# Optimization experiments

Measured on AMD Instinct MI355X. Metric: run time of the kernel, lower is better.

The kernel has to match this reference:

```python
import jax, jax.numpy as jnp
import numpy as np

N_HEADS = 32
N_KV_HEADS = 8
HEAD_DIM = 128
ROPE_BASE = 10000.0
NEG_INF = -1e9


def rope(x, base=ROPE_BASE, offset=0):
    # x: [B, H, L, d]; 'traditional' RoPE with the module's rotation formula.
    d = x.shape[-1]
    t = jnp.arange(x.shape[2], dtype=jnp.float32) + offset
    freqs = base ** (-jnp.arange(0, d, 2, dtype=jnp.float32) / d)  # [d/2]
    ang = t[:, None] * freqs[None, :]                              # [L, d/2]
    cos, sin = jnp.cos(ang), jnp.sin(ang)
    x1, x2 = x[..., 0::2], x[..., 1::2]
    out = jnp.stack([x1 * cos + x2 * sin, x1 * sin - x2 * cos], axis=-1)
    return out.reshape(x.shape)


def setup_inputs() -> dict:
    key = jax.random.key(0)
    ks = jax.random.split(key, 5)
    B, L, D = 2, 2048, 4096
    x = jax.random.normal(ks[0], (B, L, D), dtype=jnp.float32)
    wq = jax.random.normal(ks[1], (D, N_HEADS * HEAD_DIM), dtype=jnp.float32) * 0.02
    wk = jax.random.normal(ks[2], (D, N_KV_HEADS * HEAD_DIM), dtype=jnp.float32) * 0.02
    wv = jax.random.normal(ks[3], (D, N_KV_HEADS * HEAD_DIM), dtype=jnp.float32) * 0.02
    wo = jax.random.normal(ks[4], (N_HEADS * HEAD_DIM, D), dtype=jnp.float32) * 0.02
    # causal additive mask [L, L]
    mask = jnp.where(jnp.tril(jnp.ones((L, L), dtype=bool)), 0.0, NEG_INF).astype(jnp.float32)
    return {"x": x, "mask": mask, "wq": wq, "wk": wk, "wv": wv, "wo": wo}


def reference(x, mask, wq, wk, wv, wo):
    B, L, D = x.shape
    scale = HEAD_DIM ** -0.5
    q = (x @ wq).reshape(B, L, N_HEADS, HEAD_DIM).transpose(0, 2, 1, 3)     # [B,H,L,d]
    k = (x @ wk).reshape(B, L, N_KV_HEADS, HEAD_DIM).transpose(0, 2, 1, 3)  # [B,Hk,L,d]
    v = (x @ wv).reshape(B, L, N_KV_HEADS, HEAD_DIM).transpose(0, 2, 1, 3)
    rep = N_HEADS // N_KV_HEADS
    k = jnp.repeat(k, rep, axis=1)  # [B,H,L,d]  (physical GQA repeat, as in source)
    v = jnp.repeat(v, rep, axis=1)
    q = rope(q)
    k = rope(k)
    scores = jnp.einsum("bhqd,bhkd->bhqk", q * scale, k) + mask  # [B,H,L,L]
    probs = jax.nn.softmax(scores.astype(jnp.float32), axis=-1).astype(scores.dtype)
    out = jnp.einsum("bhqk,bhkd->bhqd", probs, v)
    out = out.transpose(0, 2, 1, 3).reshape(B, L, N_HEADS * HEAD_DIM)
    return out @ wo, (k, v)
```

## Files before the change

kernel.cpp:

```cpp
#include <hip/hip_runtime.h>

typedef unsigned short u16;
typedef unsigned int u32;
typedef float f32x4 __attribute__((ext_vector_type(4)));
typedef u32 u32x2 __attribute__((ext_vector_type(2)));
typedef __bf16 bf16x8 __attribute__((ext_vector_type(8)));

#define DEV __device__ __forceinline__

DEV u16 f2b(float f) {
    union { float f; u32 u; } v; v.f = f;
    u32 r = v.u + 0x7fffu + ((v.u >> 16) & 1u);
    return (u16)(r >> 16);
}
DEV float b2f(u16 b) {
    union { u32 u; float f; } v; v.u = ((u32)b) << 16;
    return v.f;
}

DEV void gload16(const void* g, void* l) {
    __builtin_amdgcn_global_load_lds((const __attribute__((address_space(1))) void*)g,
                                     (__attribute__((address_space(3))) void*)l, 16, 0, 0);
}

DEV f32x4 mfma16(bf16x8 a, bf16x8 b, f32x4 c) {
    return __builtin_amdgcn_mfma_f32_16x16x32_bf16(a, b, c, 0, 0, 0);
}

__global__ __launch_bounds__(256) void convx_kernel(const float* __restrict__ in,
                                                    u16* __restrict__ out) {
    size_t i = ((size_t)blockIdx.x * 256 + threadIdx.x) * 4;
    float4 v = *(const float4*)(in + i);
    ushort4 o; o.x = f2b(v.x); o.y = f2b(v.y); o.z = f2b(v.z); o.w = f2b(v.w);
    *(ushort4*)(out + i) = o;
}

__global__ __launch_bounds__(256) void tconv3_kernel(const float* __restrict__ wq,
                                                     const float* __restrict__ wk,
                                                     const float* __restrict__ wv,
                                                     u16* __restrict__ out) {
    __shared__ float tile[64][65];
    int t = threadIdx.x;
    int n0 = blockIdx.x * 64, k0 = blockIdx.y * 64;
    const float* src; int Ns, nl;
    if (n0 < 4096)      { src = wq; Ns = 4096; nl = n0; }
    else if (n0 < 5120) { src = wk; Ns = 1024; nl = n0 - 4096; }
    else                { src = wv; Ns = 1024; nl = n0 - 5120; }
    int r = t >> 4, c4 = (t & 15) * 4;
#pragma unroll
    for (int i = 0; i < 4; ++i) {
        float4 v = *(const float4*)(src + (size_t)(k0 + i * 16 + r) * Ns + nl + c4);
        tile[i * 16 + r][c4 + 0] = v.x; tile[i * 16 + r][c4 + 1] = v.y;
        tile[i * 16 + r][c4 + 2] = v.z; tile[i * 16 + r][c4 + 3] = v.w;
    }
    __syncthreads();
#pragma unroll
    for (int i = 0; i < 4; ++i) {
        int nn = i * 16 + r;
        ushort4 o;
        o.x = f2b(tile[c4 + 0][nn]); o.y = f2b(tile[c4 + 1][nn]);
        o.z = f2b(tile[c4 + 2][nn]); o.w = f2b(tile[c4 + 3][nn]);
        *(ushort4*)(out + (size_t)(n0 + nn) * 4096 + k0 + c4) = o;
    }
}

__global__ __launch_bounds__(256) void tconv_kernel(const float* __restrict__ in,
                                                    u16* __restrict__ out, int K, int N) {
    __shared__ float tile[64][65];
    int t = threadIdx.x;
    int n0 = blockIdx.x * 64, k0 = blockIdx.y * 64;
    int r = t >> 4, c4 = (t & 15) * 4;
#pragma unroll
    for (int i = 0; i < 4; ++i) {
        float4 v = *(const float4*)(in + (size_t)(k0 + i * 16 + r) * N + n0 + c4);
        tile[i * 16 + r][c4 + 0] = v.x; tile[i * 16 + r][c4 + 1] = v.y;
        tile[i * 16 + r][c4 + 2] = v.z; tile[i * 16 + r][c4 + 3] = v.w;
    }
    __syncthreads();
#pragma unroll
    for (int i = 0; i < 4; ++i) {
        int nn = i * 16 + r;
        ushort4 o;
        o.x = f2b(tile[c4 + 0][nn]); o.y = f2b(tile[c4 + 1][nn]);
        o.z = f2b(tile[c4 + 2][nn]); o.w = f2b(tile[c4 + 3][nn]);
        *(ushort4*)(out + (size_t)(n0 + nn) * K + k0 + c4) = o;
    }
}

#define GEMM128_BODY                                                                        \
    __shared__ __align__(16) u16 Asb[2][2][64 * 64];                                        \
    __shared__ __align__(16) u16 Bsb[2][2][64 * 64];                                        \
    int t = threadIdx.x;                                                                    \
    int lane = t & 63, w = t >> 6;                                                          \
    int wrM = w >> 1, wcN = w & 1;                                                          \
    int lr = lane & 15, hi = lane >> 4;                                                     \
    int wg = blockIdx.x;                                                                    \
    int swz = (wg & 7) * ((int)gridDim.x >> 3) + (wg >> 3);                                 \
    int bx = swz / gy, by = swz % gy;                                                       \
    int m0 = by * 128, n0 = bx * 128;                                                       \
    int nk = K >> 6;                                                                        \
    auto stageA = [&](int X, int h) {                                                       \
        const u16* src = A + (size_t)(m0 + h * 64) * K + X * 64;                            \
        char* dst = (char*)&Asb[X & 1][h][0];                                               \
        _Pragma("unroll")                                                                   \
        for (int it = 0; it < 2; ++it) {                                                    \
            int c = it * 256 + t;                                                           \
            int row = c >> 3;                                                               \
            int col8 = ((c & 7) ^ (row & 7)) << 3;                                          \
            gload16(src + (size_t)row * K + col8, dst + (it * 256 + (t & ~63)) * 16);       \
        }                                                                                   \
    };                                                                                      \
    auto stageB = [&](int X, int h) {                                                       \
        const u16* src = Bt + (size_t)(n0 + h * 64) * K + X * 64;                           \
        char* dst = (char*)&Bsb[X & 1][h][0];                                               \
        _Pragma("unroll")                                                                   \
        for (int it = 0; it < 2; ++it) {                                                    \
            int c = it * 256 + t;                                                           \
            int row = c >> 3;                                                               \
            int col8 = ((c & 7) ^ (row & 7)) << 3;                                          \
            gload16(src + (size_t)row * K + col8, dst + (it * 256 + (t & ~63)) * 16);       \
        }                                                                                   \
    };                                                                                      \
    stageA(0, 0); stageA(0, 1); stageB(0, 0); stageB(0, 1);                                 \
    stageA(1, 0); stageA(1, 1);                                                             \
    asm volatile("s_waitcnt vmcnt(4)" ::: "memory");                                        \
    __builtin_amdgcn_s_barrier();                                                           \
    f32x4 acc[4][4] = {};                                                                   \
    for (int kt = 0; kt < nk; ++kt) {                                                       \
        __builtin_amdgcn_sched_barrier(0);                                                  \
        int p = kt & 1;                                                                     \
        const char* Ah = (const char*)&Asb[p][wrM][0];                                      \
        const char* Bh = (const char*)&Bsb[p][wcN][0];                                      \
        bool s1 = (kt + 1 < nk), s2 = (kt + 2 < nk);                                        \
        bf16x8 a[4][2], bb[2][2];                                                           \
        _Pragma("unroll")                                                                   \
        for (int mf = 0; mf < 4; ++mf)                                                      \
            _Pragma("unroll")                                                               \
            for (int ks = 0; ks < 2; ++ks) {                                                \
                int row = mf * 16 + lr;                                                     \
                a[mf][ks] = *(const bf16x8*)(Ah + ((row * 128 + ks * 64 + hi * 16) ^ ((row & 7) << 4))); \
            }                                                                               \
        _Pragma("unroll")                                                                   \
        for (int nf = 0; nf < 2; ++nf)                                                      \
            _Pragma("unroll")                                                               \
            for (int ks = 0; ks < 2; ++ks) {                                                \
                int row = nf * 16 + lr;                                                     \
                bb[nf][ks] = *(const bf16x8*)(Bh + ((row * 128 + ks * 64 + hi * 16) ^ ((row & 7) << 4))); \
            }                                                                               \
        if (s1) { stageB(kt + 1, 0); stageB(kt + 1, 1); }                                   \
        __builtin_amdgcn_s_barrier();                                                       \
        __builtin_amdgcn_s_setprio(1);                                                      \
        _Pragma("unroll")                                                                   \
        for (int mf = 0; mf < 4; ++mf)                                                      \
            _Pragma("unroll")                                                               \
            for (int nf = 0; nf < 2; ++nf)                                                  \
                _Pragma("unroll")                                                           \
                for (int ks = 0; ks < 2; ++ks)                                              \
                    acc[mf][nf] = mfma16(a[mf][ks], bb[nf][ks], acc[mf][nf]);               \
        __builtin_amdgcn_s_setprio(0);                                                      \
        __builtin_amdgcn_s_barrier();                                                       \
        _Pragma("unroll")                                                                   \
        for (int nf = 0; nf < 2; ++nf)                                                      \
            _Pragma("unroll")                                                               \
            for (int ks = 0; ks < 2; ++ks) {                                                \
                int row = (nf + 2) * 16 + lr;                                               \
                bb[nf][ks] = *(const bf16x8*)(Bh + ((row * 128 + ks * 64 + hi * 16) ^ ((row & 7) << 4))); \
            }                                                                               \
        if (s2) { stageA(kt + 2, 0); stageA(kt + 2, 1); }                                   \
        __builtin_amdgcn_s_barrier();                                                       \
        __builtin_amdgcn_s_setprio(1);                                                      \
        _Pragma("unroll")                                                                   \
        for (int mf = 0; mf < 4; ++mf)                                                      \
            _Pragma("unroll")                                                               \
            for (int nf = 0; nf < 2; ++nf)                                                  \
                _Pragma("unroll")                                                           \
                for (int ks = 0; ks < 2; ++ks)                                              \
                    acc[mf][nf + 2] = mfma16(a[mf][ks], bb[nf][ks], acc[mf][nf + 2]);       \
        __builtin_amdgcn_s_setprio(0);                                                      \
        if (s2)      asm volatile("s_waitcnt vmcnt(4)" ::: "memory");                       \
        else if (s1) asm volatile("s_waitcnt vmcnt(0)" ::: "memory");                       \
        __builtin_amdgcn_s_barrier();                                                       \
    }

__global__ __launch_bounds__(256, 2) void gemm128_bf16_kernel(const u16* __restrict__ A,
                                                              const u16* __restrict__ Bt,
                                                              u16* __restrict__ Cb,
                                                              int N, int K, int gy) {
    GEMM128_BODY
#pragma unroll
    for (int mf = 0; mf < 4; ++mf)
#pragma unroll
        for (int nf = 0; nf < 4; ++nf)
#pragma unroll
            for (int r = 0; r < 4; ++r) {
                int m = m0 + wrM * 64 + mf * 16 + hi * 4 + r;
                int n = n0 + wcN * 64 + nf * 16 + lr;
                Cb[(size_t)m * N + n] = f2b(acc[mf][nf][r]);
            }
}

__global__ __launch_bounds__(256, 2) void gemm128_f32_kernel(const u16* __restrict__ A,
                                                             const u16* __restrict__ Bt,
                                                             float* __restrict__ Cf,
                                                             int N, int K, int gy) {
    GEMM128_BODY
#pragma unroll
    for (int mf = 0; mf < 4; ++mf)
#pragma unroll
        for (int nf = 0; nf < 4; ++nf)
#pragma unroll
            for (int r = 0; r < 4; ++r) {
                int m = m0 + wrM * 64 + mf * 16 + hi * 4 + r;
                int n = n0 + wcN * 64 + nf * 16 + lr;
                Cf[(size_t)m * N + n] = acc[mf][nf][r];
            }
}

__global__ __launch_bounds__(256) void postproc_kernel(u16* __restrict__ qkv,
                                                       float* __restrict__ outk,
                                                       u16* __restrict__ vt,
                                                       float* __restrict__ outv) {
    int id = blockIdx.x;
    int tid = threadIdx.x;
    if (id < 40960) {
        int row = id / 10;
        int p = (id % 10) * 256 + tid;
        int b = row >> 11, l = row & 2047;
        float freq = exp2f((float)(p & 63) * -0.2076205059304601f);
        float sv, cv; sincosf((float)l * freq, &sv, &cv);
        if (p < 2048) {
            int h = p >> 6, i = p & 63;
            size_t idx = (size_t)row * 6144 + h * 128 + 2 * i;
            u32 pr = *(const u32*)(qkv + idx);
            float x1 = b2f((u16)(pr & 0xffff)), x2 = b2f((u16)(pr >> 16));
            float o1 = x1 * cv + x2 * sv, o2 = x1 * sv - x2 * cv;
            *(u32*)(qkv + idx) = (u32)f2b(o1) | ((u32)f2b(o2) << 16);
        } else {
            int kvh = (p >> 6) - 32, i = p & 63;
            size_t idx = (size_t)row * 6144 + 4096 + kvh * 128 + 2 * i;
            u32 pr = *(const u32*)(qkv + idx);
            float x1 = b2f((u16)(pr & 0xffff)), x2 = b2f((u16)(pr >> 16));
            float o1 = x1 * cv + x2 * sv, o2 = x1 * sv - x2 * cv;
            *(u32*)(qkv + idx) = (u32)f2b(o1) | ((u32)f2b(o2) << 16);
#pragma unroll
            for (int r = 0; r < 4; ++r) {
                float2 o; o.x = o1; o.y = o2;
                *(float2*)(outk + ((size_t)((b * 32 + kvh * 4 + r) * 2048) + l) * 128 + 2 * i) = o;
            }
        }
    } else {
        __shared__ u16 tile[64][65];
        int i0 = id - 40960;
        int l0 = (i0 & 31) * 64, d0 = ((i0 >> 5) & 1) * 64;
        int z = i0 >> 6, b = z >> 3, kvh = z & 7;
        int r = tid >> 4, c4 = (tid & 15) * 4;
#pragma unroll
        for (int i = 0; i < 4; ++i) {
            int l = l0 + i * 16 + r;
            ushort4 v = *(const ushort4*)(qkv + (size_t)(b * 2048 + l) * 6144 + 5120 + kvh * 128 + d0 + c4);
            tile[i * 16 + r][c4 + 0] = v.x; tile[i * 16 + r][c4 + 1] = v.y;
            tile[i * 16 + r][c4 + 2] = v.z; tile[i * 16 + r][c4 + 3] = v.w;
            float4 f; f.x = b2f(v.x); f.y = b2f(v.y); f.z = b2f(v.z); f.w = b2f(v.w);
#pragma unroll
            for (int rr = 0; rr < 4; ++rr)
                *(float4*)(outv + ((size_t)((b * 32 + kvh * 4 + rr) * 2048) + l) * 128 + d0 + c4) = f;
        }
        __syncthreads();
#pragma unroll
        for (int i = 0; i < 4; ++i) {
            int dn = i * 16 + r;
            ushort4 o;
            o.x = tile[c4 + 0][dn]; o.y = tile[c4 + 1][dn];
            o.z = tile[c4 + 2][dn]; o.w = tile[c4 + 3][dn];
            *(ushort4*)(vt + (size_t)((b * 8 + kvh) * 128 + d0 + dn) * 2048 + l0 + c4) = o;
        }
    }
}

__global__ __launch_bounds__(256, 2) void attn_kernel(const u16* __restrict__ qkv,
                                                      const u16* __restrict__ vt,
                                                      u16* __restrict__ ab) {
    __shared__ __align__(16) u16 Kbuf[2][64 * 128];
    __shared__ __align__(16) u16 Vbuf[2][128 * 64];
    __shared__ __align__(16) u16 Ps[4][32 * 64];
    int t = threadIdx.x, lane = t & 63, w = t >> 6;
    int lr = lane & 15, hi = lane >> 4;
    int h = blockIdx.y, b = blockIdx.z, kvh = h >> 2;

    const u16* kbase = qkv + (size_t)(b * 2048) * 6144 + 4096 + kvh * 128;
    const u16* vtbase = vt + (size_t)((b * 8 + kvh) * 128) * 2048;

    auto stageKV = [&](int k0, int buf) {
#pragma unroll
        for (int i = 0; i < 4; ++i) {
            int c = i * 256 + t;
            int row = c >> 4;
            int col8 = ((c & 15) ^ (row & 7)) << 3;
            gload16(kbase + (size_t)(k0 + row) * 6144 + col8,
                    (char*)Kbuf[buf] + (i * 256 + (t & ~63)) * 16);
        }
#pragma unroll
        for (int i = 0; i < 4; ++i) {
            int c = i * 256 + t;
            int row = c >> 3;
            int col8 = ((c & 7) ^ (row & 7)) << 3;
            gload16(vtbase + (size_t)row * 2048 + k0 + col8,
                    (char*)Vbuf[buf] + (i * 256 + (t & ~63)) * 16);
        }
    };

    auto process = [&](int qblk) {
        int q0 = qblk * 128;
        bf16x8 qf[2][4];
#pragma unroll
        for (int half = 0; half < 2; ++half)
#pragma unroll
            for (int kki = 0; kki < 4; ++kki)
                qf[half][kki] = *(const bf16x8*)(qkv +
                    (size_t)(b * 2048 + q0 + w * 32 + half * 16 + lr) * 6144 + h * 128 +
                    kki * 32 + 8 * hi);
        f32x4 acc[2][8] = {};
        float mrun[2] = {-1e30f, -1e30f}, lrun[2] = {0.f, 0.f};

        int nt = 2 * (qblk + 1);
        stageKV(0, 0);
        __syncthreads();
        int cur = 0;
        for (int kt = 0; kt < nt; ++kt) {
            if (kt + 1 < nt) stageKV((kt + 1) * 64, cur ^ 1);
            __builtin_amdgcn_sched_barrier(0);

            const u16* Ks = Kbuf[cur];
            const u16* Vs = Vbuf[cur];
            f32x4 s[2][4] = {};
            __builtin_amdgcn_s_setprio(1);
#pragma unroll
            for (int kki = 0; kki < 4; ++kki) {
                bf16x8 kf[4];
#pragma unroll
                for (int fc = 0; fc < 4; ++fc) {
                    int kvr = fc * 16 + lr;
                    int byt = (kvr * 256 + (kki * 32 + 8 * hi) * 2) ^ ((kvr & 7) << 4);
                    kf[fc] = *(const bf16x8*)((const char*)Ks + byt);
                }
#pragma unroll
                for (int fc = 0; fc < 4; ++fc) {
                    s[0][fc] = mfma16(kf[fc], qf[0][kki], s[0][fc]);
                    s[1][fc] = mfma16(kf[fc], qf[1][kki], s[1][fc]);
                }
            }
            __builtin_amdgcn_s_setprio(0);
            const float SC = 0.08838834764831845f;
            int domask = (kt >= nt - 2);
            u16* Pw = Ps[w];
#pragma unroll
            for (int half = 0; half < 2; ++half) {
                int qabs = q0 + w * 32 + half * 16 + lr;
#pragma unroll
                for (int fc = 0; fc < 4; ++fc)
#pragma unroll
                    for (int r = 0; r < 4; ++r) {
                        float v = s[half][fc][r] * SC;
                        if (domask && (kt * 64 + fc * 16 + hi * 4 + r) > qabs) v = -1e30f;
                        s[half][fc][r] = v;
                    }
                float pm = s[half][0][0];
#pragma unroll
                for (int fc = 0; fc < 4; ++fc)
#pragma unroll
                    for (int r = 0; r < 4; ++r) pm = fmaxf(pm, s[half][fc][r]);
                pm = fmaxf(pm, __shfl_xor(pm, 16));
                pm = fmaxf(pm, __shfl_xor(pm, 32));
                float mn = fmaxf(mrun[half], pm);
                float fr = __expf(mrun[half] - mn);
                mrun[half] = mn;
                float ls = 0.f;
#pragma unroll
                for (int fc = 0; fc < 4; ++fc)
#pragma unroll
                    for (int r = 0; r < 4; ++r) {
                        float e = __expf(s[half][fc][r] - mn);
                        s[half][fc][r] = e;
                        ls += e;
                    }
                ls += __shfl_xor(ls, 16);
                ls += __shfl_xor(ls, 32);
                lrun[half] = lrun[half] * fr + ls;
#pragma unroll
                for (int dhf = 0; dhf < 8; ++dhf)
#pragma unroll
                    for (int r = 0; r < 4; ++r) acc[half][dhf][r] *= fr;
#pragma unroll
                for (int fc = 0; fc < 4; ++fc) {
                    u32x2 pk;
                    pk.x = (u32)f2b(s[half][fc][0]) | ((u32)f2b(s[half][fc][1]) << 16);
                    pk.y = (u32)f2b(s[half][fc][2]) | ((u32)f2b(s[half][fc][3]) << 16);
                    int byt = (half * 2048 + lr * 128 + fc * 32 + hi * 8) ^ ((lr & 7) << 4);
                    *(u32x2*)((char*)Pw + byt) = pk;
                }
            }
            asm volatile("s_waitcnt lgkmcnt(0)" ::: "memory");
            __builtin_amdgcn_s_setprio(1);
#pragma unroll
            for (int kk2 = 0; kk2 < 2; ++kk2) {
                bf16x8 pf0 = *(const bf16x8*)((const char*)Pw +
                    ((lr * 128 + kk2 * 64 + hi * 16) ^ ((lr & 7) << 4)));
                bf16x8 pf1 = *(const bf16x8*)((const char*)Pw +
                    ((2048 + lr * 128 + kk2 * 64 + hi * 16) ^ ((lr & 7) << 4)));
#pragma unroll
                for (int dhf = 0; dhf < 8; ++dhf) {
                    int dh = dhf * 16 + lr;
                    int bytv = (dh * 128 + (kk2 * 32 + 8 * hi) * 2) ^ ((dh & 7) << 4);
                    bf16x8 vf = *(const bf16x8*)((const char*)Vs + bytv);
                    acc[0][dhf] = mfma16(vf, pf0, acc[0][dhf]);
                    acc[1][dhf] = mfma16(vf, pf1, acc[1][dhf]);
                }
            }
            __builtin_amdgcn_s_setprio(0);
            __syncthreads();
            cur ^= 1;
        }
#pragma unroll
        for (int half = 0; half < 2; ++half) {
            float inv = 1.0f / lrun[half];
            int qrow = q0 + w * 32 + half * 16 + lr;
#pragma unroll
            for (int dhf = 0; dhf < 8; ++dhf) {
                ushort4 o;
                o.x = f2b(acc[half][dhf][0] * inv); o.y = f2b(acc[half][dhf][1] * inv);
                o.z = f2b(acc[half][dhf][2] * inv); o.w = f2b(acc[half][dhf][3] * inv);
                *(ushort4*)(ab + (size_t)(b * 2048 + qrow) * 4096 + h * 128 + dhf * 16 + hi * 4) = o;
            }
        }
    };

    process(15 - blockIdx.x);
    __syncthreads();
    process(blockIdx.x);
}

extern "C" void kernel_launch(void* const* d_in, const int* in_sizes, int n_in,
                              void* d_out, int out_size, void* d_ws, size_t ws_size,
                              hipStream_t stream) {
    (void)in_sizes; (void)n_in; (void)out_size; (void)ws_size;
    const float* x  = (const float*)d_in[0];
    const float* wq = (const float*)d_in[2];
    const float* wk = (const float*)d_in[3];
    const float* wv = (const float*)d_in[4];
    const float* wo = (const float*)d_in[5];

    char* ws = (char*)d_ws;
    u16* xb  = (u16*)(ws + 0);
    u16* fBt = (u16*)(ws + 33554432);
    u16* qkv = (u16*)(ws + 83886080);
    u16* vt  = (u16*)(ws + 134217728);
    u16* ab  = xb;
    u16* wob = fBt;

    float* out0 = (float*)d_out;
    float* outk = out0 + 16777216;
    float* outv = out0 + 33554432;

    convx_kernel<<<16384, 256, 0, stream>>>(x, xb);
    tconv3_kernel<<<dim3(96, 64), 256, 0, stream>>>(wq, wk, wv, fBt);

    gemm128_bf16_kernel<<<1536, 256, 0, stream>>>(xb, fBt, qkv, 6144, 4096, 32);

    tconv_kernel<<<dim3(64, 64), 256, 0, stream>>>(wo, wob, 4096, 4096);

    postproc_kernel<<<41984, 256, 0, stream>>>(qkv, outk, vt, outv);

    attn_kernel<<<dim3(8, 32, 2), 256, 0, stream>>>(qkv, vt, ab);

    gemm128_f32_kernel<<<1024, 256, 0, stream>>>(ab, wob, out0, 4096, 4096, 32);
}
```

Before: 580.9 us.

## Merge preprocessing kernels, fold softmax scale into Q RoPE, add lazy rescaling

Folds the x conversion, the QKV weight transpose and the wo transpose into one preproc kernel, which removes three launches and lets the wo conversion run before the QKV GEMM. wo gets its own workspace region so it no longer aliases fBt. The attention scale is applied to Q during RoPE postprocessing instead of per score tile. The online softmax now rescales the accumulators only when the running max grows by more than a threshold, which cuts per-tile multiplies at some risk to numeric range.

```diff
diff --git a/kernel.cpp b/kernel.cpp
--- a/kernel.cpp
+++ b/kernel.cpp
@@ -27,25 +27,36 @@
     return __builtin_amdgcn_mfma_f32_16x16x32_bf16(a, b, c, 0, 0, 0);
 }
 
-__global__ __launch_bounds__(256) void convx_kernel(const float* __restrict__ in,
-                                                    u16* __restrict__ out) {
-    size_t i = ((size_t)blockIdx.x * 256 + threadIdx.x) * 4;
-    float4 v = *(const float4*)(in + i);
-    ushort4 o; o.x = f2b(v.x); o.y = f2b(v.y); o.z = f2b(v.z); o.w = f2b(v.w);
-    *(ushort4*)(out + i) = o;
-}
-
-__global__ __launch_bounds__(256) void tconv3_kernel(const float* __restrict__ wq,
-                                                     const float* __restrict__ wk,
-                                                     const float* __restrict__ wv,
-                                                     u16* __restrict__ out) {
+__global__ __launch_bounds__(256) void preproc_kernel(const float* __restrict__ x,
+                                                      const float* __restrict__ wq,
+                                                      const float* __restrict__ wk,
+                                                      const float* __restrict__ wv,
+                                                      const float* __restrict__ wo,
+                                                      u16* __restrict__ xb,
+                                                      u16* __restrict__ fBt,
+                                                      u16* __restrict__ wob) {
+    int id = blockIdx.x;
+    int t = threadIdx.x;
+    if (id < 16384) {
+        size_t i = ((size_t)id * 256 + t) * 4;
+        float4 v = *(const float4*)(x + i);
+        ushort4 o; o.x = f2b(v.x); o.y = f2b(v.y); o.z = f2b(v.z); o.w = f2b(v.w);
+        *(ushort4*)(xb + i) = o;
+        return;
+    }
     __shared__ float tile[64][65];
-    int t = threadIdx.x;
-    int n0 = blockIdx.x * 64, k0 = blockIdx.y * 64;
-    const float* src; int Ns, nl;
-    if (n0 < 4096)      { src = wq; Ns = 4096; nl = n0; }
-    else if (n0 < 5120) { src = wk; Ns = 1024; nl = n0 - 4096; }
-    else                { src = wv; Ns = 1024; nl = n0 - 5120; }
+    const float* src; u16* dst; int Ns, nl, n0, k0, Kst;
+    if (id < 22528) {
+        int i0 = id - 16384;
+        n0 = (i0 % 96) * 64; k0 = (i0 / 96) * 64; Kst = 4096; dst = fBt;
+        if (n0 < 4096)      { src = wq; Ns = 4096; nl = n0; }
+        else if (n0 < 5120) { src = wk; Ns = 1024; nl = n0 - 4096; }
+        else                { src = wv; Ns = 1024; nl = n0 - 5120; }
+    } else {
+        int i1 = id - 22528;
+        n0 = (i1 & 63) * 64; k0 = (i1 >> 6) * 64; Kst = 4096; dst = wob;
+        src = wo; Ns = 4096; nl = n0;
+    }
     int r = t >> 4, c4 = (t & 15) * 4;
 #pragma unroll
     for (int i = 0; i < 4; ++i) {
@@ -60,30 +71,7 @@
         ushort4 o;
         o.x = f2b(tile[c4 + 0][nn]); o.y = f2b(tile[c4 + 1][nn]);
         o.z = f2b(tile[c4 + 2][nn]); o.w = f2b(tile[c4 + 3][nn]);
-        *(ushort4*)(out + (size_t)(n0 + nn) * 4096 + k0 + c4) = o;
-    }
-}
-
-__global__ __launch_bounds__(256) void tconv_kernel(const float* __restrict__ in,
-                                                    u16* __restrict__ out, int K, int N) {
-    __shared__ float tile[64][65];
-    int t = threadIdx.x;
-    int n0 = blockIdx.x * 64, k0 = blockIdx.y * 64;
-    int r = t >> 4, c4 = (t & 15) * 4;
-#pragma unroll
-    for (int i = 0; i < 4; ++i) {
-        float4 v = *(const float4*)(in + (size_t)(k0 + i * 16 + r) * N + n0 + c4);
-        tile[i * 16 + r][c4 + 0] = v.x; tile[i * 16 + r][c4 + 1] = v.y;
-        tile[i * 16 + r][c4 + 2] = v.z; tile[i * 16 + r][c4 + 3] = v.w;
-    }
-    __syncthreads();
-#pragma unroll
-    for (int i = 0; i < 4; ++i) {
-        int nn = i * 16 + r;
-        ushort4 o;
-        o.x = f2b(tile[c4 + 0][nn]); o.y = f2b(tile[c4 + 1][nn]);
-        o.z = f2b(tile[c4 + 2][nn]); o.w = f2b(tile[c4 + 3][nn]);
-        *(ushort4*)(out + (size_t)(n0 + nn) * K + k0 + c4) = o;
+        *(ushort4*)(dst + (size_t)(n0 + nn) * Kst + k0 + c4) = o;
     }
 }
 
@@ -229,11 +217,12 @@
         float freq = exp2f((float)(p & 63) * -0.2076205059304601f);
         float sv, cv; sincosf((float)l * freq, &sv, &cv);
         if (p < 2048) {
+            const float SC = 0.08838834764831845f;
             int h = p >> 6, i = p & 63;
             size_t idx = (size_t)row * 6144 + h * 128 + 2 * i;
             u32 pr = *(const u32*)(qkv + idx);
             float x1 = b2f((u16)(pr & 0xffff)), x2 = b2f((u16)(pr >> 16));
-            float o1 = x1 * cv + x2 * sv, o2 = x1 * sv - x2 * cv;
+            float o1 = (x1 * cv + x2 * sv) * SC, o2 = (x1 * sv - x2 * cv) * SC;
             *(u32*)(qkv + idx) = (u32)f2b(o1) | ((u32)f2b(o2) << 16);
         } else {
             int kvh = (p >> 6) - 32, i = p & 63;
@@ -350,20 +339,18 @@
                 }
             }
             __builtin_amdgcn_s_setprio(0);
-            const float SC = 0.08838834764831845f;
             int domask = (kt >= nt - 2);
             u16* Pw = Ps[w];
 #pragma unroll
             for (int half = 0; half < 2; ++half) {
                 int qabs = q0 + w * 32 + half * 16 + lr;
-#pragma unroll
-                for (int fc = 0; fc < 4; ++fc)
-#pragma unroll
-                    for (int r = 0; r < 4; ++r) {
-                        float v = s[half][fc][r] * SC;
-                        if (domask && (kt * 64 + fc * 16 + hi * 4 + r) > qabs) v = -1e30f;
-                        s[half][fc][r] = v;
-                    }
+                if (domask) {
+#pragma unroll
+                    for (int fc = 0; fc < 4; ++fc)
+#pragma unroll
+                        for (int r = 0; r < 4; ++r)
+                            if ((kt * 64 + fc * 16 + hi * 4 + r) > qabs) s[half][fc][r] = -1e30f;
+                }
                 float pm = s[half][0][0];
 #pragma unroll
                 for (int fc = 0; fc < 4; ++fc)
@@ -371,25 +358,28 @@
                     for (int r = 0; r < 4; ++r) pm = fmaxf(pm, s[half][fc][r]);
                 pm = fmaxf(pm, __shfl_xor(pm, 16));
                 pm = fmaxf(pm, __shfl_xor(pm, 32));
-                float mn = fmaxf(mrun[half], pm);
-                float fr = __expf(mrun[half] - mn);
-                mrun[half] = mn;
+                if (!__all(pm - mrun[half] <= 8.0f)) {
+                    float mn = fmaxf(mrun[half], pm);
+                    float fr = __expf(mrun[half] - mn);
+                    mrun[half] = mn;
+                    lrun[half] *= fr;
+#pragma unroll
+                    for (int dhf = 0; dhf < 8; ++dhf)
+#pragma unroll
+                        for (int r = 0; r < 4; ++r) acc[half][dhf][r] *= fr;
+                }
                 float ls = 0.f;
 #pragma unroll
                 for (int fc = 0; fc < 4; ++fc)
 #pragma unroll
                     for (int r = 0; r < 4; ++r) {
-                        float e = __expf(s[half][fc][r] - mn);
+                        float e = __expf(s[half][fc][r] - mrun[half]);
                         s[half][fc][r] = e;
                         ls += e;
                     }
                 ls += __shfl_xor(ls, 16);
                 ls += __shfl_xor(ls, 32);
-                lrun[half] = lrun[half] * fr + ls;
-#pragma unroll
-                for (int dhf = 0; dhf < 8; ++dhf)
-#pragma unroll
-                    for (int r = 0; r < 4; ++r) acc[half][dhf][r] *= fr;
+                lrun[half] += ls;
 #pragma unroll
                 for (int fc = 0; fc < 4; ++fc) {
                     u32x2 pk;
@@ -455,19 +445,15 @@
     u16* qkv = (u16*)(ws + 83886080);
     u16* vt  = (u16*)(ws + 134217728);
     u16* ab  = xb;
-    u16* wob = fBt;
-
+    u16* wob = (u16*)(ws + 142606336);
     float* out0 = (float*)d_out;
     float* outk = out0 + 16777216;
     float* outv = out0 + 33554432;
 
-    convx_kernel<<<16384, 256, 0, stream>>>(x, xb);
-    tconv3_kernel<<<dim3(96, 64), 256, 0, stream>>>(wq, wk, wv, fBt);
+    preproc_kernel<<<26624, 256, 0, stream>>>(x, wq, wk, wv, wo, xb, fBt, wob);
 
     gemm128_bf16_kernel<<<1536, 256, 0, stream>>>(xb, fBt, qkv, 6144, 4096, 32);
 
-    tconv_kernel<<<dim3(64, 64), 256, 0, stream>>>(wo, wob, 4096, 4096);
-
     postproc_kernel<<<41984, 256, 0, stream>>>(qkv, outk, vt, outv);
 
     attn_kernel<<<dim3(8, 32, 2), 256, 0, stream>>>(qkv, vt, ab);
```

New measurement: 603.8 us. 1.04x slower.
